# Performance work log

Hardware: AMD Instinct MI355X
Metric: run time of the kernel (lower is better)

Reference implementation:

```python
import jax, jax.numpy as jnp
import numpy as np

DOWNSAMPLE = 4
REG = 0.05
SINKHORN_ITERS = 50
LAMBDA_OT = 1.0
LAMBDA_TV = 1.0


def setup_inputs() -> dict:
    key = jax.random.key(0)
    k1, k2 = jax.random.split(key)
    pred = jax.random.uniform(k1, (16, 1, 256, 256), dtype=jnp.float32)
    gt = jax.random.uniform(k2, (16, 1, 256, 256), dtype=jnp.float32)
    return {"pred": pred, "gt": gt, "epoch": 5, "max_epoch": 10}


def _avg_pool(x, k):
    B, C, H, W = x.shape
    return x.reshape(B, C, H // k, k, W // k, k).mean(axis=(3, 5))


def _normalize(x, n):
    # relu then normalize to a distribution; fall back to uniform if sum==0
    x = jnp.maximum(x, 0.0)
    s = x.sum(axis=1, keepdims=True)  # [B,1]
    return jnp.where(s > 0, x / s, jnp.full_like(x, 1.0 / n))


def _curriculum_loss(pred, gt, epoch, max_epoch):
    B = pred.shape[0]
    # --- counting loss: L1 between total counts ---
    pc = pred.reshape(B, -1).sum(axis=1)
    gc = gt.reshape(B, -1).sum(axis=1)
    l_count = jnp.abs(pc - gc).mean()

    t = float(epoch) / float(max(1, max_epoch))
    ot_w = LAMBDA_OT * t
    tv_w = LAMBDA_TV * t

    # --- OT loss (batched Sinkhorn) ---
    pd = _avg_pool(pred, DOWNSAMPLE)
    gd = _avg_pool(gt, DOWNSAMPLE)
    h, w = pd.shape[2], pd.shape[3]
    n = h * w
    ys = jnp.arange(h, dtype=jnp.float32)
    xs = jnp.arange(w, dtype=jnp.float32)
    yy, xx = jnp.meshgrid(ys, xs, indexing="ij")
    yf = yy.reshape(-1)  # [n]
    xf = xx.reshape(-1)
    # squared euclidean cost matrix [n,n], built separably (no [n,n,2] temp)
    M = (yf[:, None] - yf[None, :]) ** 2 + (xf[:, None] - xf[None, :]) ** 2
    K = jnp.exp(-M / REG)  # [n,n]

    a = _normalize(pd.reshape(B, -1), n)  # [B,n]
    b = _normalize(gd.reshape(B, -1), n)

    def step(uv, _):
        u, v = uv
        u = a / (v @ K.T)  # K @ v per sample, batched
        v = b / (u @ K)    # K.T @ u per sample, batched
        return (u, v), None

    ones = jnp.ones((B, n), dtype=pred.dtype)
    (u, v), _ = jax.lax.scan(step, (ones, ones), None, length=SINKHORN_ITERS)
    # cost_b = sum_ij u_i K_ij v_j M_ij
    cost = jnp.einsum("bn,nm,bm->b", u, K * M, v)
    l_ot = cost.mean()

    # --- total variation loss ---
    dx = jnp.abs(pred[:, :, :, 1:] - pred[:, :, :, :-1]).mean()
    dy = jnp.abs(pred[:, :, 1:, :] - pred[:, :, :-1, :]).mean()
    l_tv = dx + dy

    return l_count + ot_w * l_ot + tv_w * l_tv


def reference(pred, gt, epoch, max_epoch):
    return _curriculum_loss(pred, gt, epoch, max_epoch)
```

## Files before the change

### kernel.cpp

```cpp
#include <hip/hip_runtime.h>
#include <math.h>


#define KW1 2.0611536224385578e-09f
#define MW2 8.4967085105831778e-18f
#define RP2 72
#define PDOFF 2048
#define GDOFF 67584

__device__ __forceinline__ float dpp_right(float x) {
  return __int_as_float(__builtin_amdgcn_update_dpp(
      0, __float_as_int(x), 0x101, 0xF, 0xF, true));
}
__device__ __forceinline__ float dpp_left(float x) {
  return __int_as_float(__builtin_amdgcn_update_dpp(
      0, __float_as_int(x), 0x111, 0xF, 0xF, true));
}
__device__ __forceinline__ float wshr1(float x) {
  return __int_as_float(__builtin_amdgcn_update_dpp(
      0, __float_as_int(x), 0x138, 0xF, 0xF, true));
}
__device__ __forceinline__ float wshl1(float x) {
  return __int_as_float(__builtin_amdgcn_update_dpp(
      0, __float_as_int(x), 0x130, 0xF, 0xF, true));
}

__device__ __forceinline__ float ad4(const float4 a, const float4 b) {
  return fabsf(a.x - b.x) + fabsf(a.y - b.y) + fabsf(a.z - b.z) + fabsf(a.w - b.w);
}
__device__ __forceinline__ float agent_ld(const float* p) {
  return __hip_atomic_load(p, __ATOMIC_RELAXED, __HIP_MEMORY_SCOPE_AGENT);
}

__global__ __launch_bounds__(256) void prep_kernel(
    const float* __restrict__ pred, const float* __restrict__ gt,
    float* __restrict__ ws, unsigned int* __restrict__ cnt) {
  __shared__ float rbuf[16];
  const int g = blockIdx.x;
  const int im = g >> 4, band = g & 15;
  const int t = threadIdx.x;
  if (g == 0 && t == 0) *cnt = 0u;
  const int ppy = t >> 6, ppx = t & 63;
  const float* pb = pred + im * 65536;
  const float* gb = gt + im * 65536;
  const int sr0 = band * 16 + ppy * 4;
  const int c0 = ppx * 4;

  float4 q[4];
  float ps = 0.f, gs = 0.f, sx = 0.f, sy = 0.f;
#pragma unroll
  for (int r = 0; r < 4; ++r) {
    q[r] = *(const float4*)(pb + (sr0 + r) * 256 + c0);
    const float4 e = *(const float4*)(gb + (sr0 + r) * 256 + c0);
    ps += (q[r].x + q[r].y) + (q[r].z + q[r].w);
    gs += (e.x + e.y) + (e.z + e.w);
    sx += fabsf(q[r].y - q[r].x) + fabsf(q[r].z - q[r].y) + fabsf(q[r].w - q[r].z);
    const float nf = __shfl_down(q[r].x, 1);
    if (ppx < 63) sx += fabsf(nf - q[r].w);
  }
  sy += ad4(q[1], q[0]) + ad4(q[2], q[1]) + ad4(q[3], q[2]);
  if (sr0 + 4 < 256) {
    const float4 qn = *(const float4*)(pb + (sr0 + 4) * 256 + c0);
    sy += ad4(qn, q[3]);
  }
  const int prow = band * 4 + ppy;
  ws[PDOFF + im * 4096 + prow * 64 + ppx] = fmaxf(ps * 0.0625f, 0.f);
  ws[GDOFF + im * 4096 + prow * 64 + ppx] = fmaxf(gs * 0.0625f, 0.f);

  float r0 = ps, r1 = gs, r2 = sx, r3 = sy;
#pragma unroll
  for (int o = 32; o > 0; o >>= 1) {
    r0 += __shfl_down(r0, o); r1 += __shfl_down(r1, o);
    r2 += __shfl_down(r2, o); r3 += __shfl_down(r3, o);
  }
  if ((t & 63) == 0) {
    const int w = t >> 6;
    rbuf[w * 4 + 0] = r0; rbuf[w * 4 + 1] = r1;
    rbuf[w * 4 + 2] = r2; rbuf[w * 4 + 3] = r3;
  }
  __syncthreads();
  if (t == 0) {
    float a0 = 0, a1 = 0, a2 = 0, a3 = 0;
    for (int w = 0; w < 4; ++w) {
      a0 += rbuf[w * 4]; a1 += rbuf[w * 4 + 1];
      a2 += rbuf[w * 4 + 2]; a3 += rbuf[w * 4 + 3];
    }
    ws[g] = a0; ws[256 + g] = a1; ws[512 + g] = a2; ws[768 + g] = a3;
  }
}

__global__ __launch_bounds__(1024) void sink_kernel(
    float* __restrict__ ws, const int* __restrict__ epoch,
    const int* __restrict__ max_epoch, float* __restrict__ out,
    unsigned int* __restrict__ cnt) {
  __shared__ float SuL[18 * 64], SuR[18 * 64], SvL[18 * 64], SvR[18 * 64];
  __shared__ float rbuf[40];
  __shared__ int lastflag;

  const int b = blockIdx.x;
  const int t = threadIdx.x;
  const int w = t >> 6;
  const int l = t & 63;

  for (int i = t; i < 18 * 64; i += 1024) {
    SuL[i] = 0.f; SuR[i] = 0.f; SvL[i] = 0.f; SvR[i] = 0.f;
  }

  float av[4], bv[4];
  const float4 qa = *(const float4*)&ws[PDOFF + b * 4096 + l * 64 + 4 * w];
  const float4 qb = *(const float4*)&ws[GDOFF + b * 4096 + l * 64 + 4 * w];
  av[0] = qa.x; av[1] = qa.y; av[2] = qa.z; av[3] = qa.w;
  bv[0] = qb.x; bv[1] = qb.y; bv[2] = qb.z; bv[3] = qb.w;
  float spd = (qa.x + qa.y) + (qa.z + qa.w);
  float sgd = (qb.x + qb.y) + (qb.z + qb.w);
#pragma unroll
  for (int o = 32; o > 0; o >>= 1) {
    spd += __shfl_down(spd, o); sgd += __shfl_down(sgd, o);
  }
  if (l == 0) { rbuf[w * 2] = spd; rbuf[w * 2 + 1] = sgd; }
  __syncthreads();
  float Sp = 0.f, Sg = 0.f;
#pragma unroll
  for (int k = 0; k < 16; ++k) { Sp += rbuf[2 * k]; Sg += rbuf[2 * k + 1]; }

#pragma unroll
  for (int j = 0; j < 4; ++j) {
    av[j] = (Sp > 0.f) ? (av[j] / Sp) : (1.f / 4096.f);
    bv[j] = (Sg > 0.f) ? (bv[j] / Sg) : (1.f / 4096.f);
  }

  const int rdL = w * 64 + l;
  const int rdR = (w + 2) * 64 + l;
  const int wr  = (w + 1) * 64 + l;

  float uu[4], vv[4] = {1.f, 1.f, 1.f, 1.f}, hh[4];
  SvL[wr] = 1.f; SvR[wr] = 1.f;
  __syncthreads();

#pragma unroll 1
  for (int it = 0; it < 50; ++it) {
    {
      const float xl = SvR[rdL];
      const float xr = SvL[rdR];
      hh[0] = fmaf(KW1, xl + vv[1], vv[0]);
      hh[1] = fmaf(KW1, vv[0] + vv[2], vv[1]);
      hh[2] = fmaf(KW1, vv[1] + vv[3], vv[2]);
      hh[3] = fmaf(KW1, vv[2] + xr, vv[3]);
#pragma unroll
      for (int c = 0; c < 4; ++c) {
        const float d = fmaf(KW1, wshr1(hh[c]) + wshl1(hh[c]), hh[c]);
        uu[c] = av[c] * __builtin_amdgcn_rcpf(d);
      }
      SuL[wr] = uu[0]; SuR[wr] = uu[3];
    }
    __syncthreads();
    {
      const float xl = SuR[rdL];
      const float xr = SuL[rdR];
      hh[0] = fmaf(KW1, xl + uu[1], uu[0]);
      hh[1] = fmaf(KW1, uu[0] + uu[2], uu[1]);
      hh[2] = fmaf(KW1, uu[1] + uu[3], uu[2]);
      hh[3] = fmaf(KW1, uu[2] + xr, uu[3]);
#pragma unroll
      for (int c = 0; c < 4; ++c) {
        const float d = fmaf(KW1, wshr1(hh[c]) + wshl1(hh[c]), hh[c]);
        vv[c] = bv[c] * __builtin_amdgcn_rcpf(d);
      }
      SvL[wr] = vv[0]; SvR[wr] = vv[3];
    }
    __syncthreads();
  }

  float c = 0.f;
  {
    const float xl = SvR[rdL];
    const float xr = SvL[rdR];
#pragma unroll
    for (int cc = 0; cc < 4; ++cc) {
      const float vl = (cc == 0) ? xl : vv[cc - 1];
      const float vr = (cc == 3) ? xr : vv[cc + 1];
      const float s = vl + vr;
      const float e = (wshr1(vv[cc]) + wshl1(vv[cc])) + s;
      const float d = wshr1(s) + wshl1(s);
      c += uu[cc] * fmaf(MW2, d, KW1 * e);
    }
  }
#pragma unroll
  for (int o = 32; o > 0; o >>= 1) c += __shfl_down(c, o);
  if (l == 0) rbuf[w] = c;
  __syncthreads();
  if (t == 0) {
    float s = 0.f;
    for (int k = 0; k < 16; ++k) s += rbuf[k];
    ws[1024 + b] = s;
    __threadfence();
    const unsigned int old = atomicAdd(cnt, 1u);
    lastflag = (old == 15u) ? 1 : 0;
  }
  __syncthreads();

  if (lastflag) {
    __threadfence();
    float myPc = 0.f, myGc = 0.f, myTx = 0.f, myTy = 0.f;
    if (t < 256) {
      myPc = agent_ld(&ws[t]);
      myGc = agent_ld(&ws[256 + t]);
      myTx = agent_ld(&ws[512 + t]);
      myTy = agent_ld(&ws[768 + t]);
    }
#pragma unroll
    for (int o = 8; o > 0; o >>= 1) {
      myPc += __shfl_down(myPc, o, 16);
      myGc += __shfl_down(myGc, o, 16);
    }
    float d = ((t & 15) == 0) ? fabsf(myPc - myGc) : 0.f;
    float ct = (t < 16) ? agent_ld(&ws[1024 + t]) : 0.f;
#pragma unroll
    for (int o = 32; o > 0; o >>= 1) {
      d += __shfl_down(d, o); ct += __shfl_down(ct, o);
      myTx += __shfl_down(myTx, o); myTy += __shfl_down(myTy, o);
    }
    if ((t & 63) == 0 && t < 256) {
      const int ww = t >> 6;
      rbuf[16 + ww * 4] = d; rbuf[16 + ww * 4 + 1] = ct;
      rbuf[16 + ww * 4 + 2] = myTx; rbuf[16 + ww * 4 + 3] = myTy;
    }
    __syncthreads();
    if (t == 0) {
      float lc = 0, lot = 0, tvx = 0, tvy = 0;
      for (int ww = 0; ww < 4; ++ww) {
        lc += rbuf[16 + ww * 4]; lot += rbuf[16 + ww * 4 + 1];
        tvx += rbuf[16 + ww * 4 + 2]; tvy += rbuf[16 + ww * 4 + 3];
      }
      int me = max_epoch[0]; if (me < 1) me = 1;
      const float tt = (float)epoch[0] / (float)me;
      const float ltv = tvx / (16.f * 256.f * 255.f) + tvy / (16.f * 255.f * 256.f);
      out[0] = lc * (1.f / 16.f) + tt * (lot * (1.f / 16.f)) + tt * ltv;
    }
  }
}

__device__ __forceinline__ void hrow4(const float f[4], float h[4]) {
  const float l = dpp_left(f[3]);
  const float r = dpp_right(f[0]);
  h[0] = fmaf(KW1, l + f[1], f[0]);
  h[1] = fmaf(KW1, f[0] + f[2], f[1]);
  h[2] = fmaf(KW1, f[1] + f[3], f[2]);
  h[3] = fmaf(KW1, f[2] + r, f[3]);
}
__device__ __forceinline__ void phase_core(
    const float prev[4][4], float ph[4][4],
    const float cf0[4], const float cf3[4],
    float2 mA, float4 mB, float2 mC, float2 pA, float4 pB, float2 pC,
    float* __restrict__ RT_wr, float* __restrict__ RB_wr, int wb,
    float out0[4], float out3[4]) {
  hrow4(prev[0], ph[0]); hrow4(prev[1], ph[1]);
  hrow4(prev[2], ph[2]); hrow4(prev[3], ph[3]);
  float hm[4], hp[4];
  hm[0] = fmaf(KW1, mA.y + mB.y, mB.x);
  hm[1] = fmaf(KW1, mB.x + mB.z, mB.y);
  hm[2] = fmaf(KW1, mB.y + mB.w, mB.z);
  hm[3] = fmaf(KW1, mB.z + mC.x, mB.w);
  hp[0] = fmaf(KW1, pA.y + pB.y, pB.x);
  hp[1] = fmaf(KW1, pB.x + pB.z, pB.y);
  hp[2] = fmaf(KW1, pB.y + pB.w, pB.z);
  hp[3] = fmaf(KW1, pB.z + pC.x, pB.w);
#pragma unroll
  for (int j = 0; j < 4; ++j)
    out0[j] = cf0[j] * __builtin_amdgcn_rcpf(fmaf(KW1, hm[j] + ph[1][j], ph[0][j]));
#pragma unroll
  for (int j = 0; j < 4; ++j)
    out3[j] = cf3[j] * __builtin_amdgcn_rcpf(fmaf(KW1, ph[2][j] + hp[j], ph[3][j]));
  *(float4*)&RT_wr[wb] = make_float4(out0[0], out0[1], out0[2], out0[3]);
  *(float4*)&RB_wr[wb] = make_float4(out3[0], out3[1], out3[2], out3[3]);
}

__global__ __launch_bounds__(256) void fused_fallback(
    const float* __restrict__ pred, const float* __restrict__ gt,
    float* __restrict__ ws, const int* __restrict__ epoch,
    const int* __restrict__ max_epoch, float* __restrict__ out,
    unsigned int* __restrict__ cnt) {
  __shared__ float RTu[18 * RP2], RBu[18 * RP2];
  __shared__ float RTv[18 * RP2], RBv[18 * RP2];
  __shared__ float rbuf[24];

  const int b = blockIdx.x;
  const int t = threadIdx.x;
  const int tyg = t >> 4, tx = t & 15;
  const int y0 = tyg * 4, x0 = tx * 4;

  for (int i = t; i < 18 * RP2; i += 256) {
    RTu[i] = 0.f; RBu[i] = 0.f; RTv[i] = 0.f; RBv[i] = 0.f;
  }

  const float* pb = pred + b * 65536;
  const float* gb = gt + b * 65536;
  const int sr0 = 4 * y0, sc0 = 4 * x0;

  float pd[4][4], gd[4][4];
  float4 pr0, pr1, pr2, pr3;
  float spraw = 0.f, sgraw = 0.f, sx = 0.f, sy = 0.f;
#pragma unroll
  for (int i = 0; i < 4; ++i) {
    float a0 = 0.f, a1 = 0.f, a2 = 0.f, a3 = 0.f;
    float c0 = 0.f, c1 = 0.f, c2 = 0.f, c3 = 0.f;
#pragma unroll 1
    for (int rr = 0; rr < 4; ++rr) {
      const int r = i * 4 + rr;
      const float* prow = pb + (sr0 + r) * 256 + sc0;
      const float4 q0 = *(const float4*)(prow);
      const float4 q1 = *(const float4*)(prow + 4);
      const float4 q2 = *(const float4*)(prow + 8);
      const float4 q3 = *(const float4*)(prow + 12);
      const float s0 = (q0.x + q0.y) + (q0.z + q0.w);
      const float s1 = (q1.x + q1.y) + (q1.z + q1.w);
      const float s2 = (q2.x + q2.y) + (q2.z + q2.w);
      const float s3 = (q3.x + q3.y) + (q3.z + q3.w);
      a0 += s0; a1 += s1; a2 += s2; a3 += s3;
      spraw += (s0 + s1) + (s2 + s3);
      sx += fabsf(q0.y - q0.x) + fabsf(q0.z - q0.y) + fabsf(q0.w - q0.z)
          + fabsf(q1.x - q0.w)
          + fabsf(q1.y - q1.x) + fabsf(q1.z - q1.y) + fabsf(q1.w - q1.z)
          + fabsf(q2.x - q1.w)
          + fabsf(q2.y - q2.x) + fabsf(q2.z - q2.y) + fabsf(q2.w - q2.z)
          + fabsf(q3.x - q2.w)
          + fabsf(q3.y - q3.x) + fabsf(q3.z - q3.y) + fabsf(q3.w - q3.z);
      const float nf = dpp_right(q0.x);
      if (tx < 15) sx += fabsf(nf - q3.w);
      if (r > 0) sy += ad4(q0, pr0) + ad4(q1, pr1) + ad4(q2, pr2) + ad4(q3, pr3);
      pr0 = q0; pr1 = q1; pr2 = q2; pr3 = q3;
      const float* grow = gb + (sr0 + r) * 256 + sc0;
      const float4 g0 = *(const float4*)(grow);
      const float4 g1 = *(const float4*)(grow + 4);
      const float4 g2 = *(const float4*)(grow + 8);
      const float4 g3 = *(const float4*)(grow + 12);
      const float u0 = (g0.x + g0.y) + (g0.z + g0.w);
      const float u1 = (g1.x + g1.y) + (g1.z + g1.w);
      const float u2 = (g2.x + g2.y) + (g2.z + g2.w);
      const float u3 = (g3.x + g3.y) + (g3.z + g3.w);
      c0 += u0; c1 += u1; c2 += u2; c3 += u3;
      sgraw += (u0 + u1) + (u2 + u3);
    }
    pd[i][0] = a0; pd[i][1] = a1; pd[i][2] = a2; pd[i][3] = a3;
    gd[i][0] = c0; gd[i][1] = c1; gd[i][2] = c2; gd[i][3] = c3;
  }
  if (tyg < 15) {
    const float* prow = pb + (sr0 + 16) * 256 + sc0;
    sy += ad4(*(const float4*)(prow), pr0) + ad4(*(const float4*)(prow + 4), pr1)
        + ad4(*(const float4*)(prow + 8), pr2) + ad4(*(const float4*)(prow + 12), pr3);
  }

  float spd = 0.f, sgd = 0.f;
#pragma unroll
  for (int i = 0; i < 4; ++i)
#pragma unroll
    for (int j = 0; j < 4; ++j) {
      pd[i][j] = fmaxf(pd[i][j] * 0.0625f, 0.f); spd += pd[i][j];
      gd[i][j] = fmaxf(gd[i][j] * 0.0625f, 0.f); sgd += gd[i][j];
    }

  float r0 = spraw, r1 = sgraw, r2 = spd, r3 = sgd, r4 = sx, r5 = sy;
#pragma unroll
  for (int o = 32; o > 0; o >>= 1) {
    r0 += __shfl_down(r0, o); r1 += __shfl_down(r1, o);
    r2 += __shfl_down(r2, o); r3 += __shfl_down(r3, o);
    r4 += __shfl_down(r4, o); r5 += __shfl_down(r5, o);
  }
  if ((t & 63) == 0) {
    const int w = t >> 6;
    rbuf[w * 6 + 0] = r0; rbuf[w * 6 + 1] = r1; rbuf[w * 6 + 2] = r2;
    rbuf[w * 6 + 3] = r3; rbuf[w * 6 + 4] = r4; rbuf[w * 6 + 5] = r5;
  }
  __syncthreads();
  if (t == 0) {
    float a0 = 0, a1 = 0, a2 = 0, a3 = 0, a4 = 0, a5 = 0;
    for (int w = 0; w < 4; ++w) {
      a0 += rbuf[w * 6 + 0]; a1 += rbuf[w * 6 + 1]; a2 += rbuf[w * 6 + 2];
      a3 += rbuf[w * 6 + 3]; a4 += rbuf[w * 6 + 4]; a5 += rbuf[w * 6 + 5];
    }
    ws[b] = a0; ws[16 + b] = a1; ws[48 + b] = a4; ws[64 + b] = a5;
    rbuf[0] = a2; rbuf[1] = a3;
  }
  __syncthreads();
  const float Sp = rbuf[0], Sg = rbuf[1];

  float av[4][4], bv[4][4];
#pragma unroll
  for (int i = 0; i < 4; ++i)
#pragma unroll
    for (int j = 0; j < 4; ++j) {
      av[i][j] = (Sp > 0.f) ? (pd[i][j] / Sp) : (1.f / 4096.f);
      bv[i][j] = (Sg > 0.f) ? (gd[i][j] / Sg) : (1.f / 4096.f);
    }

  const int rbb = tyg * RP2 + x0 + 2;
  const int rtb = (tyg + 2) * RP2 + x0 + 2;
  const int wb  = (1 + tyg) * RP2 + 4 + x0;

  float uu[4][4], vv[4][4], uh[4][4], vh[4][4];
#pragma unroll
  for (int i = 0; i < 4; ++i)
#pragma unroll
    for (int j = 0; j < 4; ++j) vv[i][j] = 1.f;
  *(float4*)&RTv[wb] = make_float4(1.f, 1.f, 1.f, 1.f);
  *(float4*)&RBv[wb] = make_float4(1.f, 1.f, 1.f, 1.f);
  __syncthreads();

#pragma unroll 1
  for (int it = 0; it < 50; ++it) {
    {
      const float2 mA = *(const float2*)&RBv[rbb];
      const float4 mB = *(const float4*)&RBv[rbb + 2];
      const float2 mC = *(const float2*)&RBv[rbb + 6];
      const float2 pA = *(const float2*)&RTv[rtb];
      const float4 pB = *(const float4*)&RTv[rtb + 2];
      const float2 pC = *(const float2*)&RTv[rtb + 6];
      if (it != 0) {
#pragma unroll
        for (int j = 0; j < 4; ++j) {
          vv[1][j] = bv[1][j] * __builtin_amdgcn_rcpf(fmaf(KW1, uh[0][j] + uh[2][j], uh[1][j]));
          vv[2][j] = bv[2][j] * __builtin_amdgcn_rcpf(fmaf(KW1, uh[1][j] + uh[3][j], uh[2][j]));
        }
      }
      phase_core(vv, vh, av[0], av[3], mA, mB, mC, pA, pB, pC,
                 RTu, RBu, wb, uu[0], uu[3]);
    }
    __syncthreads();
    {
      const float2 mA = *(const float2*)&RBu[rbb];
      const float4 mB = *(const float4*)&RBu[rbb + 2];
      const float2 mC = *(const float2*)&RBu[rbb + 6];
      const float2 pA = *(const float2*)&RTu[rtb];
      const float4 pB = *(const float4*)&RTu[rtb + 2];
      const float2 pC = *(const float2*)&RTu[rtb + 6];
#pragma unroll
      for (int j = 0; j < 4; ++j) {
        uu[1][j] = av[1][j] * __builtin_amdgcn_rcpf(fmaf(KW1, vh[0][j] + vh[2][j], vh[1][j]));
        uu[2][j] = av[2][j] * __builtin_amdgcn_rcpf(fmaf(KW1, vh[1][j] + vh[3][j], vh[2][j]));
      }
      phase_core(uu, uh, bv[0], bv[3], mA, mB, mC, pA, pB, pC,
                 RTv, RBv, wb, vv[0], vv[3]);
    }
    __syncthreads();
  }
#pragma unroll
  for (int j = 0; j < 4; ++j) {
    vv[1][j] = bv[1][j] * __builtin_amdgcn_rcpf(fmaf(KW1, uh[0][j] + uh[2][j], uh[1][j]));
    vv[2][j] = bv[2][j] * __builtin_amdgcn_rcpf(fmaf(KW1, uh[1][j] + uh[3][j], uh[2][j]));
  }

  float c = 0.f;
  {
    const float2 mA = *(const float2*)&RBv[rbb];
    const float4 mB = *(const float4*)&RBv[rbb + 2];
    const float2 mC = *(const float2*)&RBv[rbb + 6];
    const float2 pA = *(const float2*)&RTv[rtb];
    const float4 pB = *(const float4*)&RTv[rtb + 2];
    const float2 pC = *(const float2*)&RTv[rtb + 6];
    float W[6][6];
    W[0][0] = mA.y; W[0][1] = mB.x; W[0][2] = mB.y;
    W[0][3] = mB.z; W[0][4] = mB.w; W[0][5] = mC.x;
    W[5][0] = pA.y; W[5][1] = pB.x; W[5][2] = pB.y;
    W[5][3] = pB.z; W[5][4] = pB.w; W[5][5] = pC.x;
#pragma unroll
    for (int i = 0; i < 4; ++i) {
      W[1 + i][0] = dpp_left(vv[i][3]);
      W[1 + i][5] = dpp_right(vv[i][0]);
#pragma unroll
      for (int j = 0; j < 4; ++j) W[1 + i][1 + j] = vv[i][j];
    }
#pragma unroll
    for (int i = 0; i < 4; ++i)
#pragma unroll
      for (int j = 0; j < 4; ++j) {
        const float e = (W[i][j + 1] + W[i + 2][j + 1])
                      + (W[i + 1][j] + W[i + 1][j + 2]);
        const float d = (W[i][j] + W[i][j + 2])
                      + (W[i + 2][j] + W[i + 2][j + 2]);
        c += uu[i][j] * fmaf(MW2, d, KW1 * e);
      }
  }
#pragma unroll
  for (int o = 32; o > 0; o >>= 1) c += __shfl_down(c, o);
  if ((t & 63) == 0) rbuf[t >> 6] = c;
  __syncthreads();
  if (t == 0) {
    ws[32 + b] = rbuf[0] + rbuf[1] + rbuf[2] + rbuf[3];
    __threadfence();
    const unsigned int old = atomicAdd(cnt, 1u);
    if (old == 15u) {
      __threadfence();
      float lc = 0.f, lot = 0.f, tvx = 0.f, tvy = 0.f;
      for (int k = 0; k < 16; ++k) {
        const float p = agent_ld(&ws[k]);
        const float g = agent_ld(&ws[16 + k]);
        const float ct = agent_ld(&ws[32 + k]);
        const float x = agent_ld(&ws[48 + k]);
        const float y = agent_ld(&ws[64 + k]);
        lc += fabsf(p - g); lot += ct; tvx += x; tvy += y;
      }
      int me = max_epoch[0]; if (me < 1) me = 1;
      const float tt = (float)epoch[0] / (float)me;
      const float ltv = tvx / (16.f * 256.f * 255.f) + tvy / (16.f * 255.f * 256.f);
      out[0] = lc * (1.f / 16.f) + tt * (lot * (1.f / 16.f)) + tt * ltv;
    }
  }
}

extern "C" void kernel_launch(void* const* d_in, const int* in_sizes, int n_in,
                              void* d_out, int out_size, void* d_ws, size_t ws_size,
                              hipStream_t stream) {
  const float* pred = (const float*)d_in[0];
  const float* gt   = (const float*)d_in[1];
  const int* epoch  = (const int*)d_in[2];
  const int* max_ep = (const int*)d_in[3];
  float* out = (float*)d_out;
  float* ws  = (float*)d_ws;

  if (ws_size >= 600000) {
    unsigned int* cnt = (unsigned int*)((char*)d_ws + 4160);
    prep_kernel<<<dim3(256), dim3(256), 0, stream>>>(pred, gt, ws, cnt);
    sink_kernel<<<dim3(16), dim3(1024), 0, stream>>>(ws, epoch, max_ep, out, cnt);
  } else {
    unsigned int* cnt = (unsigned int*)((char*)d_ws + 384);
    hipMemsetAsync(cnt, 0, 4, stream);
    fused_fallback<<<dim3(16), dim3(256), 0, stream>>>(pred, gt, ws, epoch,
                                                       max_ep, out, cnt);
  }
}
```

Baseline: 100.3 us.

## Replace Sinkhorn block barriers with neighbor-wave LDS flags and double buffering

The Sinkhorn kernel now runs with 512 threads per image instead of 1024, so each thread handles 8 columns instead of 4. The two __syncthreads per iteration are replaced with point-to-point acquire/release flags in LDS. Each wave waits only on its two neighbouring waves, and the halo buffers are double-buffered by iteration parity so writers do not overwrite data a neighbour is still reading. The aim is to cut full-block barrier cost and let waves drift relative to each other. The trade-off is spin-wait polling and more register pressure per thread.

```diff
diff --git a/kernel.cpp b/kernel.cpp
--- a/kernel.cpp
+++ b/kernel.cpp
@@ -30,6 +30,12 @@
 }
 __device__ __forceinline__ float agent_ld(const float* p) {
   return __hip_atomic_load(p, __ATOMIC_RELAXED, __HIP_MEMORY_SCOPE_AGENT);
+}
+__device__ __forceinline__ unsigned flag_acq(const unsigned* p) {
+  return __hip_atomic_load(p, __ATOMIC_ACQUIRE, __HIP_MEMORY_SCOPE_WORKGROUP);
+}
+__device__ __forceinline__ void flag_rel(unsigned* p, unsigned v) {
+  __hip_atomic_store(p, v, __ATOMIC_RELEASE, __HIP_MEMORY_SCOPE_WORKGROUP);
 }
 
 __global__ __launch_bounds__(256) void prep_kernel(
@@ -89,11 +95,12 @@
   }
 }
 
-__global__ __launch_bounds__(1024) void sink_kernel(
+__global__ __launch_bounds__(512) void sink_kernel(
     float* __restrict__ ws, const int* __restrict__ epoch,
     const int* __restrict__ max_epoch, float* __restrict__ out,
     unsigned int* __restrict__ cnt) {
-  __shared__ float SuL[18 * 64], SuR[18 * 64], SvL[18 * 64], SvR[18 * 64];
+  __shared__ float SuL[1280], SuR[1280], SvL[1280], SvR[1280];
+  __shared__ unsigned FLu[10], FLv[10];
   __shared__ float rbuf[40];
   __shared__ int lastflag;
 
@@ -102,83 +109,105 @@
   const int w = t >> 6;
   const int l = t & 63;
 
-  for (int i = t; i < 18 * 64; i += 1024) {
+  for (int i = t; i < 1280; i += 512) {
     SuL[i] = 0.f; SuR[i] = 0.f; SvL[i] = 0.f; SvR[i] = 0.f;
   }
-
-  float av[4], bv[4];
-  const float4 qa = *(const float4*)&ws[PDOFF + b * 4096 + l * 64 + 4 * w];
-  const float4 qb = *(const float4*)&ws[GDOFF + b * 4096 + l * 64 + 4 * w];
-  av[0] = qa.x; av[1] = qa.y; av[2] = qa.z; av[3] = qa.w;
-  bv[0] = qb.x; bv[1] = qb.y; bv[2] = qb.z; bv[3] = qb.w;
-  float spd = (qa.x + qa.y) + (qa.z + qa.w);
-  float sgd = (qb.x + qb.y) + (qb.z + qb.w);
+  if (t < 10) {
+    const unsigned guard = (t == 0 || t == 9) ? 0xFFFFFFFFu : 0u;
+    FLu[t] = guard ? guard : 0u;
+    FLv[t] = guard ? guard : 1u;
+  }
+
+  float av[8], bv[8];
+  {
+    const float* P = &ws[PDOFF + b * 4096 + l * 64 + 8 * w];
+    const float* G = &ws[GDOFF + b * 4096 + l * 64 + 8 * w];
+    const float4 a0 = *(const float4*)(P);
+    const float4 a1 = *(const float4*)(P + 4);
+    const float4 b0 = *(const float4*)(G);
+    const float4 b1 = *(const float4*)(G + 4);
+    av[0] = a0.x; av[1] = a0.y; av[2] = a0.z; av[3] = a0.w;
+    av[4] = a1.x; av[5] = a1.y; av[6] = a1.z; av[7] = a1.w;
+    bv[0] = b0.x; bv[1] = b0.y; bv[2] = b0.z; bv[3] = b0.w;
+    bv[4] = b1.x; bv[5] = b1.y; bv[6] = b1.z; bv[7] = b1.w;
+  }
+  float spd = 0.f, sgd = 0.f;
+#pragma unroll
+  for (int j = 0; j < 8; ++j) { spd += av[j]; sgd += bv[j]; }
 #pragma unroll
   for (int o = 32; o > 0; o >>= 1) {
     spd += __shfl_down(spd, o); sgd += __shfl_down(sgd, o);
   }
   if (l == 0) { rbuf[w * 2] = spd; rbuf[w * 2 + 1] = sgd; }
-  __syncthreads();
+
+  const int own = (w + 1) * 64 + l;
+  SvL[own] = 1.f; SvR[own] = 1.f;
+  __syncthreads();
+
   float Sp = 0.f, Sg = 0.f;
 #pragma unroll
-  for (int k = 0; k < 16; ++k) { Sp += rbuf[2 * k]; Sg += rbuf[2 * k + 1]; }
-
-#pragma unroll
-  for (int j = 0; j < 4; ++j) {
+  for (int k = 0; k < 8; ++k) { Sp += rbuf[2 * k]; Sg += rbuf[2 * k + 1]; }
+#pragma unroll
+  for (int j = 0; j < 8; ++j) {
     av[j] = (Sp > 0.f) ? (av[j] / Sp) : (1.f / 4096.f);
     bv[j] = (Sg > 0.f) ? (bv[j] / Sg) : (1.f / 4096.f);
   }
 
   const int rdL = w * 64 + l;
   const int rdR = (w + 2) * 64 + l;
-  const int wr  = (w + 1) * 64 + l;
-
-  float uu[4], vv[4] = {1.f, 1.f, 1.f, 1.f}, hh[4];
-  SvL[wr] = 1.f; SvR[wr] = 1.f;
-  __syncthreads();
+
+  float uu[8], vv[8], hh[8];
+#pragma unroll
+  for (int j = 0; j < 8; ++j) vv[j] = 1.f;
 
 #pragma unroll 1
   for (int it = 0; it < 50; ++it) {
+    const unsigned tgt = (unsigned)it + 1u;
+    const int p = (it & 1) * 640;
     {
-      const float xl = SvR[rdL];
-      const float xr = SvL[rdR];
+      while (flag_acq(&FLv[w]) < tgt || flag_acq(&FLv[w + 2]) < tgt) {}
+      const float xl = SvR[p + rdL];
+      const float xr = SvL[p + rdR];
       hh[0] = fmaf(KW1, xl + vv[1], vv[0]);
-      hh[1] = fmaf(KW1, vv[0] + vv[2], vv[1]);
-      hh[2] = fmaf(KW1, vv[1] + vv[3], vv[2]);
-      hh[3] = fmaf(KW1, vv[2] + xr, vv[3]);
-#pragma unroll
-      for (int c = 0; c < 4; ++c) {
+#pragma unroll
+      for (int c = 1; c < 7; ++c) hh[c] = fmaf(KW1, vv[c - 1] + vv[c + 1], vv[c]);
+      hh[7] = fmaf(KW1, vv[6] + xr, vv[7]);
+#pragma unroll
+      for (int c = 0; c < 8; ++c) {
         const float d = fmaf(KW1, wshr1(hh[c]) + wshl1(hh[c]), hh[c]);
         uu[c] = av[c] * __builtin_amdgcn_rcpf(d);
       }
-      SuL[wr] = uu[0]; SuR[wr] = uu[3];
-    }
-    __syncthreads();
+      SuL[p + own] = uu[0]; SuR[p + own] = uu[7];
+      if (l == 0) flag_rel(&FLu[w + 1], tgt);
+    }
     {
-      const float xl = SuR[rdL];
-      const float xr = SuL[rdR];
+      while (flag_acq(&FLu[w]) < tgt || flag_acq(&FLu[w + 2]) < tgt) {}
+      const float xl = SuR[p + rdL];
+      const float xr = SuL[p + rdR];
       hh[0] = fmaf(KW1, xl + uu[1], uu[0]);
-      hh[1] = fmaf(KW1, uu[0] + uu[2], uu[1]);
-      hh[2] = fmaf(KW1, uu[1] + uu[3], uu[2]);
-      hh[3] = fmaf(KW1, uu[2] + xr, uu[3]);
-#pragma unroll
-      for (int c = 0; c < 4; ++c) {
+#pragma unroll
+      for (int c = 1; c < 7; ++c) hh[c] = fmaf(KW1, uu[c - 1] + uu[c + 1], uu[c]);
+      hh[7] = fmaf(KW1, uu[6] + xr, uu[7]);
+#pragma unroll
+      for (int c = 0; c < 8; ++c) {
         const float d = fmaf(KW1, wshr1(hh[c]) + wshl1(hh[c]), hh[c]);
         vv[c] = bv[c] * __builtin_amdgcn_rcpf(d);
       }
-      SvL[wr] = vv[0]; SvR[wr] = vv[3];
-    }
-    __syncthreads();
-  }
+      const int p2 = ((it + 1) & 1) * 640;
+      SvL[p2 + own] = vv[0]; SvR[p2 + own] = vv[7];
+      if (l == 0) flag_rel(&FLv[w + 1], tgt + 1u);
+    }
+  }
+  __syncthreads();
 
   float c = 0.f;
   {
     const float xl = SvR[rdL];
     const float xr = SvL[rdR];
 #pragma unroll
-    for (int cc = 0; cc < 4; ++cc) {
+    for (int cc = 0; cc < 8; ++cc) {
       const float vl = (cc == 0) ? xl : vv[cc - 1];
-      const float vr = (cc == 3) ? xr : vv[cc + 1];
+      const float vr = (cc == 7) ? xr : vv[cc + 1];
       const float s = vl + vr;
       const float e = (wshr1(vv[cc]) + wshl1(vv[cc])) + s;
       const float d = wshr1(s) + wshl1(s);
@@ -187,11 +216,11 @@
   }
 #pragma unroll
   for (int o = 32; o > 0; o >>= 1) c += __shfl_down(c, o);
-  if (l == 0) rbuf[w] = c;
+  if (l == 0) rbuf[16 + w] = c;
   __syncthreads();
   if (t == 0) {
     float s = 0.f;
-    for (int k = 0; k < 16; ++k) s += rbuf[k];
+    for (int k = 0; k < 8; ++k) s += rbuf[16 + k];
     ws[1024 + b] = s;
     __threadfence();
     const unsigned int old = atomicAdd(cnt, 1u);
@@ -222,15 +251,15 @@
     }
     if ((t & 63) == 0 && t < 256) {
       const int ww = t >> 6;
-      rbuf[16 + ww * 4] = d; rbuf[16 + ww * 4 + 1] = ct;
-      rbuf[16 + ww * 4 + 2] = myTx; rbuf[16 + ww * 4 + 3] = myTy;
+      rbuf[24 + ww * 4] = d; rbuf[24 + ww * 4 + 1] = ct;
+      rbuf[24 + ww * 4 + 2] = myTx; rbuf[24 + ww * 4 + 3] = myTy;
     }
     __syncthreads();
     if (t == 0) {
       float lc = 0, lot = 0, tvx = 0, tvy = 0;
       for (int ww = 0; ww < 4; ++ww) {
-        lc += rbuf[16 + ww * 4]; lot += rbuf[16 + ww * 4 + 1];
-        tvx += rbuf[16 + ww * 4 + 2]; tvy += rbuf[16 + ww * 4 + 3];
+        lc += rbuf[24 + ww * 4]; lot += rbuf[24 + ww * 4 + 1];
+        tvx += rbuf[24 + ww * 4 + 2]; tvy += rbuf[24 + ww * 4 + 3];
       }
       int me = max_epoch[0]; if (me < 1) me = 1;
       const float tt = (float)epoch[0] / (float)me;
@@ -520,7 +549,7 @@
   if (ws_size >= 600000) {
     unsigned int* cnt = (unsigned int*)((char*)d_ws + 4160);
     prep_kernel<<<dim3(256), dim3(256), 0, stream>>>(pred, gt, ws, cnt);
-    sink_kernel<<<dim3(16), dim3(1024), 0, stream>>>(ws, epoch, max_ep, out, cnt);
+    sink_kernel<<<dim3(16), dim3(512), 0, stream>>>(ws, epoch, max_ep, out, cnt);
   } else {
     unsigned int* cnt = (unsigned int*)((char*)d_ws + 384);
     hipMemsetAsync(cnt, 0, 4, stream);
```

New measurement: 108.1 us. 7.8% more time.
